# Performance work log

Hardware: AMD Instinct MI355X
Metric: run time of the kernel (lower is better)

The kernel has to match this reference:

```python
import jax, jax.numpy as jnp
import numpy as np

NUM_CLASSES = 50000
NUM_SAMPLED = 1000
D_MODEL = 1024
BATCH, SEQ = 32, 512


def _log_expected_count(ids, num_sampled, num_classes):
    # TF log-uniform candidate sampler (unique=True):
    # P(c) = log((c+2)/(c+1)) / log(num_classes+1)
    # E[count] = -expm1(num_sampled * log1p(-P))
    ids_f = ids.astype(jnp.float32)
    p = (jnp.log(ids_f + 2.0) - jnp.log(ids_f + 1.0)) / np.float32(np.log(num_classes + 1.0))
    return jnp.log(-jnp.expm1(num_sampled * jnp.log1p(-p)))


def setup_inputs() -> dict:
    key = jax.random.key(0)
    k1, k2, k3, k4 = jax.random.split(key, 4)
    lstm_outputs = jax.random.normal(k1, (BATCH, SEQ, D_MODEL), dtype=jnp.float32)
    next_token_ids = jax.random.randint(k2, (BATCH, SEQ), 0, NUM_CLASSES)
    sampled_ids = jax.random.randint(k3, (BATCH, NUM_SAMPLED), 0, NUM_CLASSES)
    W = jax.random.normal(k4, (NUM_CLASSES, D_MODEL), dtype=jnp.float32) * (1.0 / np.sqrt(D_MODEL))
    b = jnp.zeros((NUM_CLASSES,), dtype=jnp.float32)
    return {"lstm_outputs": lstm_outputs, "next_token_ids": next_token_ids,
            "sampled_ids": sampled_ids, "W": W, "b": b}


def reference(lstm_outputs, next_token_ids, sampled_ids, W, b):
    # Vectorized sampled-softmax loss (tf.nn.sampled_softmax_loss with
    # log-uniform sampler, partition_strategy irrelevant, accidental-hit removal),
    # mapped over the batch dim as the original tf.map_fn does.
    log_q_true = _log_expected_count(next_token_ids, NUM_SAMPLED, NUM_CLASSES)   # [B,T]
    log_q_samp = _log_expected_count(sampled_ids, NUM_SAMPLED, NUM_CLASSES)      # [B,S]

    w_true = W[next_token_ids]                                                   # [B,T,D]
    true_logit = (jnp.einsum('btd,btd->bt', lstm_outputs, w_true)
                  + b[next_token_ids] - log_q_true)                              # [B,T]

    w_samp = W[sampled_ids]                                                      # [B,S,D]
    samp_logits = (jnp.einsum('btd,bsd->bts', lstm_outputs, w_samp)
                   + b[sampled_ids][:, None, :] - log_q_samp[:, None, :])        # [B,T,S]

    # remove accidental hits (sampled id == true label)
    hit = sampled_ids[:, None, :] == next_token_ids[:, :, None]                  # [B,T,S]
    samp_logits = jnp.where(hit, jnp.float32(-1e9), samp_logits)

    all_logits = jnp.concatenate([true_logit[..., None], samp_logits], axis=-1)  # [B,T,1+S]
    # softmax CE with true class at index 0
    losses = jax.nn.logsumexp(all_logits, axis=-1) - true_logit                  # [B,T]
    return 0.5 * jnp.mean(losses)
```

## Files before the change

kernel.cpp:

```cpp
#include <hip/hip_runtime.h>
#include <cmath>

#define BATCH 32
#define SEQLEN 512
#define NSAMP 1000
#define DMODEL 1024
#define NCHUNK 4

typedef __bf16 bf16x8_t __attribute__((ext_vector_type(8)));
typedef float f32x4_t __attribute__((ext_vector_type(4)));

__device__ __forceinline__ unsigned pack_bf2(float lo, float hi) {
    unsigned ulo = __float_as_uint(lo);
    unsigned uhi = __float_as_uint(hi);
    ulo = (ulo + 0x7fffu + ((ulo >> 16) & 1u)) >> 16;
    uhi = (uhi + 0x7fffu + ((uhi >> 16) & 1u)) & 0xffff0000u;
    return (ulo & 0xffffu) | uhi;
}

__device__ __forceinline__ float log_expected_count(int id) {
    float idf = (float)id;
    float p = log1pf(1.0f / (idf + 1.0f)) * 0.09242316f;
    return logf(-expm1f(1000.0f * log1pf(-p)));
}

__device__ __forceinline__ void gl16(const void* g, void* l) {
    __builtin_amdgcn_global_load_lds(
        (const __attribute__((address_space(1))) unsigned int*)g,
        (__attribute__((address_space(3))) unsigned int*)l,
        16, 0, 0);
}

__global__ __launch_bounds__(256) void prep_kernel(
    const float* __restrict__ h, const int* __restrict__ labels,
    const int* __restrict__ sids, const float* __restrict__ W,
    const float* __restrict__ bias, unsigned short* __restrict__ Wb,
    unsigned short* __restrict__ hb,
    float* __restrict__ adjw, float* __restrict__ tlw)
{
    const int w = threadIdx.x >> 6, lane = threadIdx.x & 63;
    if (blockIdx.x < 8000) {
        const int row = blockIdx.x * 4 + w;
        const int sv = sids[row];
        const float4* src = (const float4*)(W + (size_t)sv * DMODEL);
        unsigned short* dst = Wb + (size_t)row * DMODEL;
#pragma unroll
        for (int j = 0; j < 4; ++j) {
            float4 v = src[lane + j * 64];
            uint2 u;
            u.x = pack_bf2(v.x, v.y);
            u.y = pack_bf2(v.z, v.w);
            *(uint2*)(dst + (lane + j * 64) * 4) = u;
        }
        if (lane == 0) adjw[row] = bias[sv] - log_expected_count(sv);
    } else {
        const int r = (blockIdx.x - 8000) * 4 + w;
        const int lab = labels[r];
        const float4* hp = (const float4*)(h + (size_t)r * DMODEL);
        const float4* wp = (const float4*)(W + (size_t)lab * DMODEL);
        unsigned short* hdst = hb + (size_t)r * DMODEL;
        float s = 0.0f;
#pragma unroll
        for (int j = 0; j < 4; ++j) {
            float4 a = hp[lane + j * 64];
            float4 c = wp[lane + j * 64];
            s += a.x * c.x + a.y * c.y + a.z * c.z + a.w * c.w;
            uint2 u;
            u.x = pack_bf2(a.x, a.y);
            u.y = pack_bf2(a.z, a.w);
            *(uint2*)(hdst + (lane + j * 64) * 4) = u;
        }
#pragma unroll
        for (int off = 32; off > 0; off >>= 1) s += __shfl_xor(s, off, 64);
        if (lane == 0) tlw[r] = s + bias[lab] - log_expected_count(lab);
    }
}

__global__ __launch_bounds__(256, 3) void sampled_softmax_main(
    const int* __restrict__ labels, const int* __restrict__ sids,
    const unsigned short* __restrict__ hb, const unsigned short* __restrict__ Wb,
    const float* __restrict__ adjw,
    float* __restrict__ pm, float* __restrict__ pl)
{
    __shared__ __align__(16) unsigned short Ab[2][64 * 32];
    __shared__ __align__(16) unsigned short Bb[2][256 * 32];
    __shared__ int   sid_lds[256];
    __shared__ float adj_lds[256];
    __shared__ int   lab_lds[64];
    __shared__ float mpart[4][64];
    __shared__ float lpart[4][64];

    const int bb     = blockIdx.x;
    const int chunk  = blockIdx.y;
    const int tile_t = blockIdx.z;
    const int t0  = tile_t * 64;
    const int tid = threadIdx.x;
    const int w   = tid >> 6, l = tid & 63;
    const int lm  = l & 15,   q = l >> 4;
    const int rl4 = l >> 2,  cp = l & 3;

    {
        const int s = chunk * 256 + tid;
        const bool v = s < NSAMP;
        sid_lds[tid] = v ? sids[bb * NSAMP + s] : -1;
        adj_lds[tid] = v ? adjw[bb * NSAMP + s] : 0.0f;
        if (tid < 64) lab_lds[tid] = labels[bb * SEQLEN + t0 + tid];
    }

    const int swzs = (rl4 & 3) ^ ((rl4 >> 2) & 3);
    const int cs = (cp ^ swzs) * 8;
    const unsigned short* aS = hb + (size_t)(bb * SEQLEN + t0 + 16 * w + rl4) * DMODEL + cs;
    const unsigned short* bS[4];
#pragma unroll
    for (int j = 0; j < 4; ++j) {
        int rb = chunk * 256 + 64 * w + 16 * j + rl4;
        if (rb > NSAMP - 1) rb = NSAMP - 1;
        bS[j] = Wb + (size_t)(bb * NSAMP + rb) * DMODEL + cs;
    }

    const int fswz = (lm & 3) ^ ((lm >> 2) & 3);
    const int fp = (q ^ fswz) * 8;
    int aoff[4], boff[4];
#pragma unroll
    for (int t = 0; t < 4; ++t) aoff[t] = (16 * t + lm) * 32 + fp;
#pragma unroll
    for (int c = 0; c < 4; ++c) boff[c] = (64 * w + 16 * c + lm) * 32 + fp;

    f32x4_t acc[4][4];
#pragma unroll
    for (int t = 0; t < 4; ++t)
#pragma unroll
        for (int c = 0; c < 4; ++c) acc[t][c] = (f32x4_t){0.f, 0.f, 0.f, 0.f};

    gl16(aS, &Ab[0][(16 * w) * 32]);
#pragma unroll
    for (int j = 0; j < 4; ++j) gl16(bS[j], &Bb[0][(64 * w + 16 * j) * 32]);
    __syncthreads();

    for (int kt = 0; kt < 32; ++kt) {
        const int cur = kt & 1;
        if (kt + 1 < 32) {
            const int adv = (kt + 1) * 32;
            gl16(aS + adv, &Ab[cur ^ 1][(16 * w) * 32]);
#pragma unroll
            for (int j = 0; j < 4; ++j)
                gl16(bS[j] + adv, &Bb[cur ^ 1][(64 * w + 16 * j) * 32]);
        }
        const unsigned short* Ac = Ab[cur];
        const unsigned short* Bc = Bb[cur];
        bf16x8_t fa[4];
#pragma unroll
        for (int t = 0; t < 4; ++t) fa[t] = *(const bf16x8_t*)(Ac + aoff[t]);
#pragma unroll
        for (int c = 0; c < 4; ++c) {
            bf16x8_t fb = *(const bf16x8_t*)(Bc + boff[c]);
#pragma unroll
            for (int t = 0; t < 4; ++t)
                acc[t][c] = __builtin_amdgcn_mfma_f32_16x16x32_bf16(fa[t], fb, acc[t][c], 0, 0, 0);
        }
        __syncthreads();
    }

    float adjv[4]; int sidv[4]; bool cval[4];
#pragma unroll
    for (int c = 0; c < 4; ++c) {
        const int col = 64 * w + 16 * c + lm;
        adjv[c] = adj_lds[col];
        sidv[c] = sid_lds[col];
        cval[c] = (chunk * 256 + col) < NSAMP;
    }
#pragma unroll
    for (int t = 0; t < 4; ++t) {
#pragma unroll
        for (int i = 0; i < 4; ++i) {
            const int r = 16 * t + 4 * q + i;
            const int lab = lab_lds[r];
            float x[4]; bool ok[4];
            float m = -INFINITY;
#pragma unroll
            for (int c = 0; c < 4; ++c) {
                x[c] = acc[t][c][i] + adjv[c];
                ok[c] = cval[c] && (sidv[c] != lab);
                if (ok[c]) m = fmaxf(m, x[c]);
            }
            float ls = 0.0f;
#pragma unroll
            for (int c = 0; c < 4; ++c) ls += ok[c] ? __expf(x[c] - m) : 0.0f;
#pragma unroll
            for (int off = 1; off < 16; off <<= 1) {
                const float mo = __shfl_xor(m, off, 64);
                const float lo = __shfl_xor(ls, off, 64);
                const float M  = fmaxf(m, mo);
                const float e1 = (ls > 0.0f) ? ls * __expf(m - M) : 0.0f;
                const float e2 = (lo > 0.0f) ? lo * __expf(mo - M) : 0.0f;
                m = M; ls = e1 + e2;
            }
            if (lm == 0) { mpart[w][r] = m; lpart[w][r] = ls; }
        }
    }
    __syncthreads();
    if (tid < 64) {
        float m = -INFINITY, lsum = 0.0f;
#pragma unroll
        for (int p = 0; p < 4; ++p) {
            const float mp = mpart[p][tid];
            const float lp = lpart[p][tid];
            if (lp > 0.0f) {
                if (mp > m) { lsum = lsum * __expf(m - mp) + lp; m = mp; }
                else        { lsum += lp * __expf(mp - m); }
            }
        }
        const int idx = (bb * SEQLEN + t0 + tid) * NCHUNK + chunk;
        pm[idx] = m;
        pl[idx] = lsum;
    }
}

__global__ __launch_bounds__(256) void combine_kernel(
    const float* __restrict__ pm, const float* __restrict__ pl,
    const float* __restrict__ tlw, float* __restrict__ bsum)
{
    __shared__ float wsum[4];
    const int tid = threadIdx.x;
    const int w = tid >> 6, lane = tid & 63;
    const int idx = blockIdx.x * 256 + tid;
    float m = -INFINITY, l = 0.0f;
#pragma unroll
    for (int c = 0; c < NCHUNK; ++c) {
        const float mp = pm[idx * NCHUNK + c];
        const float lp = pl[idx * NCHUNK + c];
        if (lp > 0.0f) {
            if (mp > m) { l = l * __expf(m - mp) + lp; m = mp; }
            else        { l += lp * __expf(mp - m); }
        }
    }
    const float t = tlw[idx];
    const float M = fmaxf(m, t);
    float loss = __logf(l * __expf(m - M) + __expf(t - M)) + M - t;
#pragma unroll
    for (int off = 32; off > 0; off >>= 1) loss += __shfl_xor(loss, off, 64);
    if (lane == 0) wsum[w] = loss;
    __syncthreads();
    if (tid == 0) bsum[blockIdx.x] = wsum[0] + wsum[1] + wsum[2] + wsum[3];
}

__global__ void finalize_kernel(const float* __restrict__ bsum, float* __restrict__ out) {
    float v = bsum[threadIdx.x];
#pragma unroll
    for (int off = 32; off > 0; off >>= 1) v += __shfl_xor(v, off, 64);
    if (threadIdx.x == 0) out[0] = v * (0.5f / (float)(BATCH * SEQLEN));
}

extern "C" void kernel_launch(void* const* d_in, const int* in_sizes, int n_in,
                              void* d_out, int out_size, void* d_ws, size_t ws_size,
                              hipStream_t stream) {
    const float* h      = (const float*)d_in[0];
    const int*   labels = (const int*)d_in[1];
    const int*   sids   = (const int*)d_in[2];
    const float* W      = (const float*)d_in[3];
    const float* bias   = (const float*)d_in[4];

    char* base = (char*)d_ws;
    unsigned short* Wb = (unsigned short*)base;
    unsigned short* hb = (unsigned short*)(base + 65536000);
    float* adjw = (float*)(base + 99090432);
    float* tlw  = (float*)(base + 99218432);
    float* pmw  = (float*)(base + 99283968);
    float* plw  = (float*)(base + 99546112);
    float* bsum = (float*)(base + 99808256);

    prep_kernel<<<dim3(12096), dim3(256), 0, stream>>>(h, labels, sids, W, bias, Wb, hb, adjw, tlw);
    sampled_softmax_main<<<dim3(32, NCHUNK, 8), dim3(256), 0, stream>>>(
        labels, sids, hb, Wb, adjw, pmw, plw);
    combine_kernel<<<dim3(64), dim3(256), 0, stream>>>(pmw, plw, tlw, bsum);
    finalize_kernel<<<dim3(1), dim3(64), 0, stream>>>(bsum, (float*)d_out);
}
```

Measured before the change: 410.2 us.

## Triple-buffer LDS tiles with vmcnt-based waits and single barrier per step

Moves the main GEMM loop from double to triple buffering of the A and B LDS tiles, prefetching two k-steps ahead. The full __syncthreads pair is replaced by an explicit s_waitcnt vmcnt(5) and one s_barrier per iteration, so loads stay in flight across iterations. The loop is fully unrolled, all B fragments are loaded up front, and the MFMA block is wrapped in s_setprio. The extra LDS buffer and the lower launch-bounds occupancy hint (3 to 2) trade waves per CU for deeper prefetch, and the hand-counted vmcnt relies on exactly five outstanding loads per stage.

```diff
diff --git a/kernel.cpp b/kernel.cpp
--- a/kernel.cpp
+++ b/kernel.cpp
@@ -76,14 +76,14 @@
     }
 }
 
-__global__ __launch_bounds__(256, 3) void sampled_softmax_main(
+__global__ __launch_bounds__(256, 2) void sampled_softmax_main(
     const int* __restrict__ labels, const int* __restrict__ sids,
     const unsigned short* __restrict__ hb, const unsigned short* __restrict__ Wb,
     const float* __restrict__ adjw,
     float* __restrict__ pm, float* __restrict__ pl)
 {
-    __shared__ __align__(16) unsigned short Ab[2][64 * 32];
-    __shared__ __align__(16) unsigned short Bb[2][256 * 32];
+    __shared__ __align__(16) unsigned short Ab[3][64 * 32];
+    __shared__ __align__(16) unsigned short Bb[3][256 * 32];
     __shared__ int   sid_lds[256];
     __shared__ float adj_lds[256];
     __shared__ int   lab_lds[64];
@@ -118,6 +118,16 @@
         bS[j] = Wb + (size_t)(bb * NSAMP + rb) * DMODEL + cs;
     }
 
+#define STAGE_TILE(KT, BUF)                                                   \
+    do {                                                                      \
+        const int _adv = (KT) * 32;                                           \
+        gl16(aS + _adv, &Ab[BUF][(16 * w) * 32]);                             \
+        gl16(bS[0] + _adv, &Bb[BUF][(64 * w) * 32]);                          \
+        gl16(bS[1] + _adv, &Bb[BUF][(64 * w + 16) * 32]);                     \
+        gl16(bS[2] + _adv, &Bb[BUF][(64 * w + 32) * 32]);                     \
+        gl16(bS[3] + _adv, &Bb[BUF][(64 * w + 48) * 32]);                     \
+    } while (0)
+
     const int fswz = (lm & 3) ^ ((lm >> 2) & 3);
     const int fp = (q ^ fswz) * 8;
     int aoff[4], boff[4];
@@ -132,34 +142,35 @@
 #pragma unroll
         for (int c = 0; c < 4; ++c) acc[t][c] = (f32x4_t){0.f, 0.f, 0.f, 0.f};
 
-    gl16(aS, &Ab[0][(16 * w) * 32]);
-#pragma unroll
-    for (int j = 0; j < 4; ++j) gl16(bS[j], &Bb[0][(64 * w + 16 * j) * 32]);
-    __syncthreads();
-
+    STAGE_TILE(0, 0);
+    STAGE_TILE(1, 1);
+    asm volatile("s_waitcnt lgkmcnt(0)" ::: "memory");
+    __builtin_amdgcn_s_barrier();
+
+#pragma unroll
     for (int kt = 0; kt < 32; ++kt) {
-        const int cur = kt & 1;
-        if (kt + 1 < 32) {
-            const int adv = (kt + 1) * 32;
-            gl16(aS + adv, &Ab[cur ^ 1][(16 * w) * 32]);
-#pragma unroll
-            for (int j = 0; j < 4; ++j)
-                gl16(bS[j] + adv, &Bb[cur ^ 1][(64 * w + 16 * j) * 32]);
-        }
-        const unsigned short* Ac = Ab[cur];
-        const unsigned short* Bc = Bb[cur];
+        if (kt < 31) { asm volatile("s_waitcnt vmcnt(5)" ::: "memory"); }
+        else         { asm volatile("s_waitcnt vmcnt(0)" ::: "memory"); }
+        __builtin_amdgcn_s_barrier();
+        if (kt + 2 < 32) STAGE_TILE(kt + 2, (kt + 2) % 3);
+
+        const unsigned short* Ac = Ab[kt % 3];
+        const unsigned short* Bc = Bb[kt % 3];
         bf16x8_t fa[4];
 #pragma unroll
         for (int t = 0; t < 4; ++t) fa[t] = *(const bf16x8_t*)(Ac + aoff[t]);
-#pragma unroll
-        for (int c = 0; c < 4; ++c) {
-            bf16x8_t fb = *(const bf16x8_t*)(Bc + boff[c]);
+        bf16x8_t fb[4];
+#pragma unroll
+        for (int c = 0; c < 4; ++c) fb[c] = *(const bf16x8_t*)(Bc + boff[c]);
+        __builtin_amdgcn_s_setprio(1);
+#pragma unroll
+        for (int c = 0; c < 4; ++c)
 #pragma unroll
             for (int t = 0; t < 4; ++t)
-                acc[t][c] = __builtin_amdgcn_mfma_f32_16x16x32_bf16(fa[t], fb, acc[t][c], 0, 0, 0);
-        }
-        __syncthreads();
-    }
+                acc[t][c] = __builtin_amdgcn_mfma_f32_16x16x32_bf16(fa[t], fb[c], acc[t][c], 0, 0, 0);
+        __builtin_amdgcn_s_setprio(0);
+    }
+#undef STAGE_TILE
 
     float adjv[4]; int sidv[4]; bool cval[4];
 #pragma unroll
```

Result: no change. 407.7 us (-0.6%).
